# Performance work log

Hardware: AMD Instinct MI355X
Metric: run time of the kernel (lower is better)

Reference implementation:

```python
import jax, jax.numpy as jnp
import numpy as np

N, E, D = 100000, 1600000, 128
EPS = 1e-5


def _bn(h, g, b):
    m = h.mean(0)
    v = ((h - m) ** 2).mean(0)  # biased var, as torch BatchNorm1d normalization
    return g * (h - m) / jnp.sqrt(v + EPS) + b


def _sage(x, src, dst, w_self, w_neigh, b, n):
    # mean aggregation over in-neighbors (edges src->dst)
    agg = jax.ops.segment_sum(x[src], dst, num_segments=n)          # [N, D]
    cnt = jax.ops.segment_sum(jnp.ones(src.shape, x.dtype), dst, num_segments=n)
    mean = agg / jnp.maximum(cnt, 1.0)[:, None]
    return x @ w_self + mean @ w_neigh + b


def setup_inputs() -> dict:
    key = jax.random.key(0)
    ks = jax.random.split(key, 8)
    s = 1.0 / np.sqrt(D)
    return {
        "x": jax.random.normal(ks[0], (N, D), jnp.float32),
        "src": jax.random.randint(ks[1], (E,), 0, N, jnp.int32),
        "dst": jax.random.randint(ks[2], (E,), 0, N, jnp.int32),
        "w_self1": jax.random.normal(ks[3], (D, D), jnp.float32) * s,
        "w_neigh1": jax.random.normal(ks[4], (D, D), jnp.float32) * s,
        "b1": jnp.zeros((D,), jnp.float32),
        "w_self2": jax.random.normal(ks[5], (D, D), jnp.float32) * s,
        "w_neigh2": jax.random.normal(ks[6], (D, D), jnp.float32) * s,
        "b2": jnp.zeros((D,), jnp.float32),
        "w_skip": jax.random.normal(ks[7], (D, D), jnp.float32) * s,
        "b_skip": jnp.zeros((D,), jnp.float32),
        "g1": jnp.ones((D,), jnp.float32), "be1": jnp.zeros((D,), jnp.float32),
        "g2": jnp.ones((D,), jnp.float32), "be2": jnp.zeros((D,), jnp.float32),
        "g3": jnp.ones((D,), jnp.float32), "be3": jnp.zeros((D,), jnp.float32),
    }


def reference(x, src, dst, w_self1, w_neigh1, b1, w_self2, w_neigh2, b2,
              w_skip, b_skip, g1, be1, g2, be2, g3, be3):
    n = x.shape[0]
    h1 = _sage(x, src, dst, w_self1, w_neigh1, b1, n)
    h1 = jax.nn.relu(_bn(h1, g1, be1))           # dropout: eval-mode identity
    h2 = _sage(h1, src, dst, w_self2, w_neigh2, b2, n)
    h2 = _bn(h2, g2, be2)
    skip = _bn(h1 @ w_skip + b_skip, g3, be3)
    return jax.nn.relu(h2 + skip)
```

## Files before the change

### kernel.cpp

```cpp
#include <hip/hip_runtime.h>

#define D 128
#define PCHUNK 4096
#define SCAP 8192

typedef short bf16x8 __attribute__((ext_vector_type(8)));
typedef float f32x4 __attribute__((ext_vector_type(4)));

__device__ __forceinline__ ushort f2b(float f){
  unsigned u = __builtin_bit_cast(unsigned, f);
  u += 0x7fffu + ((u >> 16) & 1u);
  return (ushort)(u >> 16);
}
__device__ __forceinline__ float b2f(ushort h){
  unsigned u = ((unsigned)h) << 16;
  return __builtin_bit_cast(float, u);
}

__global__ __launch_bounds__(256) void k_p0(const int* __restrict__ dst,
                                            int* __restrict__ bcnt, int E){
  __shared__ int h[512];
  for (int u=threadIdx.x; u<512; u+=256) h[u]=0;
  __syncthreads();
  for (long long i=(long long)blockIdx.x*256+threadIdx.x; i<E; i+=(long long)gridDim.x*256)
    atomicAdd(&h[dst[i]>>8], 1);
  __syncthreads();
  for (int u=threadIdx.x; u<512; u+=256) if (h[u]) atomicAdd(&bcnt[u], h[u]);
}

__global__ void k_bscan(const int* __restrict__ bcnt, int* __restrict__ bbase,
                        int* __restrict__ bcur, int nb, int E){
  __shared__ int sh[1024];
  int t = threadIdx.x;
  int v = (t<nb) ? bcnt[t] : 0;
  sh[t]=v; __syncthreads();
  for (int off=1; off<1024; off<<=1){
    int add = (t>=off)?sh[t-off]:0;
    __syncthreads();
    sh[t]+=add;
    __syncthreads();
  }
  if (t<nb){ int e=sh[t]-v; bbase[t]=e; bcur[t]=e; }
  if (t==nb) bbase[t]=E;
}

__global__ __launch_bounds__(256) void k_part(const int* __restrict__ src,
        const int* __restrict__ dst, int* __restrict__ bcur,
        int2* __restrict__ pairs, int E){
  __shared__ int hist[512], offA[512], offB[512], gbase[512];
  __shared__ int sS[PCHUNK], sD[PCHUNK];
  const int t = threadIdx.x;
  const int base = blockIdx.x * PCHUNK;
  const int cnt = min(PCHUNK, E - base);
  for (int u=t; u<512; u+=256) hist[u]=0;
  __syncthreads();
  int rs[16], rd[16];
  #pragma unroll
  for (int j=0;j<16;j++){
    int li = j*256 + t;
    if (li < cnt){
      rs[j]=src[base+li]; rd[j]=dst[base+li];
      atomicAdd(&hist[rd[j]>>8],1);
    } else { rs[j]=0; rd[j]=-1; }
  }
  __syncthreads();
  int *cur=offA, *nxt=offB;
  for (int u=t; u<512; u+=256) cur[u]=hist[u];
  __syncthreads();
  for (int off=1; off<512; off<<=1){
    for (int u=t; u<512; u+=256) nxt[u] = cur[u] + ((u>=off)?cur[u-off]:0);
    __syncthreads();
    int* tmp=cur; cur=nxt; nxt=tmp;
  }
  for (int u=t; u<512; u+=256) nxt[u] = cur[u]-hist[u];
  __syncthreads();
  #pragma unroll
  for (int j=0;j<16;j++){
    if (j*256+t < cnt){
      int b = rd[j]>>8;
      int p = atomicAdd(&nxt[b],1);
      sS[p]=rs[j]; sD[p]=rd[j];
    }
  }
  __syncthreads();
  for (int u=t; u<512; u+=256){
    int c = hist[u];
    if (c>0) gbase[u] = atomicAdd(&bcur[u], c);
  }
  __syncthreads();
  #pragma unroll
  for (int j=0;j<16;j++){
    int idx = j*256+t;
    if (idx<cnt){
      int d = sD[idx]; int b = d>>8;
      int gpos = gbase[b] + (idx - (cur[b]-hist[b]));
      pairs[gpos] = make_int2(sS[idx], d);
    }
  }
}

__global__ __launch_bounds__(256) void k_sortb(const int2* __restrict__ pairs,
        const int* __restrict__ bbase, int* __restrict__ offs,
        int* __restrict__ slots, int N, int NB){
  __shared__ int nh[256], nc[256], sc[256];
  __shared__ int stage[SCAP];
  const int b = blockIdx.x, t = threadIdx.x;
  const int base = bbase[b];
  const int cnt  = bbase[b+1] - base;
  nh[t]=0; __syncthreads();
  for (int i=t;i<cnt;i+=256) atomicAdd(&nh[pairs[base+i].y & 255],1);
  __syncthreads();
  int v = nh[t];
  sc[t]=v; __syncthreads();
  for (int off=1; off<256; off<<=1){
    int add = (t>=off)?sc[t-off]:0;
    __syncthreads();
    sc[t]+=add;
    __syncthreads();
  }
  int excl = sc[t]-v;
  nc[t]=excl;
  int node = (b<<8)+t;
  if (node<N) offs[node]=base+excl;
  if (b==NB-1 && t==0) offs[N]=bbase[NB];
  __syncthreads();
  if (cnt<=SCAP){
    for (int i=t;i<cnt;i+=256){
      int2 p = pairs[base+i];
      int pos = atomicAdd(&nc[p.y & 255],1);
      stage[pos]=p.x;
    }
    __syncthreads();
    for (int i=t;i<cnt;i+=256) slots[base+i]=stage[i];
  } else {
    for (int i=t;i<cnt;i+=256){
      int2 p = pairs[base+i];
      int pos = atomicAdd(&nc[p.y & 255],1);
      slots[base+pos]=p.x;
    }
  }
}

__global__ __launch_bounds__(256) void k_xcast(const float* __restrict__ x,
                                               ushort* __restrict__ xb, long long n4){
  long long i = (long long)blockIdx.x*256 + threadIdx.x;
  const long long stride = (long long)gridDim.x*256;
  for (; i < n4; i += stride){
    float4 v = reinterpret_cast<const float4*>(x)[i];
    ushort4 o;
    o.x = f2b(v.x); o.y = f2b(v.y); o.z = f2b(v.z); o.w = f2b(v.w);
    reinterpret_cast<ushort4*>(xb)[i] = o;
  }
}

__global__ void k_wt(const float* __restrict__ W, ushort* __restrict__ Wb, int K, int k0){
  int idx = blockIdx.x*256 + threadIdx.x;
  int k = idx >> 7, c = idx & 127;
  Wb[(size_t)c*K + k0 + k] = f2b(W[idx]);
}

__global__ __launch_bounds__(256) void k_gatherb(const ushort* __restrict__ Xb,
        const int* __restrict__ slots, const int* __restrict__ offs,
        ushort* __restrict__ meanb, int N){
  int node = blockIdx.x*4 + (threadIdx.x >> 6);
  int c2 = (threadIdx.x & 63) * 2;
  if (node >= N) return;
  const int beg = offs[node], end = offs[node+1];
  float sx0=0,sy0=0,sx1=0,sy1=0,sx2=0,sy2=0,sx3=0,sy3=0;
  int j = beg;
  while (j < end && (j & 3)){
    unsigned u = *reinterpret_cast<const unsigned*>(&Xb[(size_t)slots[j]*D + c2]);
    sx0 += b2f((ushort)u); sy0 += b2f((ushort)(u>>16));
    ++j;
  }
  const int nfull = (end - j) >> 2;
  const int4* sp = reinterpret_cast<const int4*>(slots + j);

#define G8(ia, ib) { \
    unsigned u0 = *reinterpret_cast<const unsigned*>(&Xb[(size_t)(ia).x*D + c2]); \
    unsigned u1 = *reinterpret_cast<const unsigned*>(&Xb[(size_t)(ia).y*D + c2]); \
    unsigned u2 = *reinterpret_cast<const unsigned*>(&Xb[(size_t)(ia).z*D + c2]); \
    unsigned u3 = *reinterpret_cast<const unsigned*>(&Xb[(size_t)(ia).w*D + c2]); \
    unsigned u4 = *reinterpret_cast<const unsigned*>(&Xb[(size_t)(ib).x*D + c2]); \
    unsigned u5 = *reinterpret_cast<const unsigned*>(&Xb[(size_t)(ib).y*D + c2]); \
    unsigned u6 = *reinterpret_cast<const unsigned*>(&Xb[(size_t)(ib).z*D + c2]); \
    unsigned u7 = *reinterpret_cast<const unsigned*>(&Xb[(size_t)(ib).w*D + c2]); \
    sx0 += b2f((ushort)u0); sy0 += b2f((ushort)(u0>>16)); \
    sx1 += b2f((ushort)u1); sy1 += b2f((ushort)(u1>>16)); \
    sx2 += b2f((ushort)u2); sy2 += b2f((ushort)(u2>>16)); \
    sx3 += b2f((ushort)u3); sy3 += b2f((ushort)(u3>>16)); \
    sx0 += b2f((ushort)u4); sy0 += b2f((ushort)(u4>>16)); \
    sx1 += b2f((ushort)u5); sy1 += b2f((ushort)(u5>>16)); \
    sx2 += b2f((ushort)u6); sy2 += b2f((ushort)(u6>>16)); \
    sx3 += b2f((ushort)u7); sy3 += b2f((ushort)(u7>>16)); }

  int g = 0;
  if (nfull >= 2){
    int4 ia = sp[0], ib = sp[1];
    for (g = 2; g + 2 <= nfull; g += 2){
      int4 na = sp[g], nb = sp[g+1];
      G8(ia, ib);
      ia = na; ib = nb;
    }
    G8(ia, ib);
  }
  if (g < nfull){
    int4 ia = sp[g];
    unsigned u0 = *reinterpret_cast<const unsigned*>(&Xb[(size_t)ia.x*D + c2]);
    unsigned u1 = *reinterpret_cast<const unsigned*>(&Xb[(size_t)ia.y*D + c2]);
    unsigned u2 = *reinterpret_cast<const unsigned*>(&Xb[(size_t)ia.z*D + c2]);
    unsigned u3 = *reinterpret_cast<const unsigned*>(&Xb[(size_t)ia.w*D + c2]);
    sx0 += b2f((ushort)u0); sy0 += b2f((ushort)(u0>>16));
    sx1 += b2f((ushort)u1); sy1 += b2f((ushort)(u1>>16));
    sx2 += b2f((ushort)u2); sy2 += b2f((ushort)(u2>>16));
    sx3 += b2f((ushort)u3); sy3 += b2f((ushort)(u3>>16));
  }
  j += 4*nfull;
  for (; j < end; ++j){
    unsigned u = *reinterpret_cast<const unsigned*>(&Xb[(size_t)slots[j]*D + c2]);
    sx0 += b2f((ushort)u); sy0 += b2f((ushort)(u>>16));
  }
#undef G8
  float deg = (float)(end - beg);
  float rc = deg > 0.f ? 1.0f/deg : 0.f;
  unsigned o = (unsigned)f2b((sx0+sx1+sx2+sx3)*rc)
             | ((unsigned)f2b((sy0+sy1+sy2+sy3)*rc) << 16);
  *reinterpret_cast<unsigned*>(&meanb[(size_t)node*D + c2]) = o;
}

template<bool SKIP>
__global__ __launch_bounds__(256, 2) void k_mfma(
    const ushort* __restrict__ A0, const ushort* __restrict__ A1,
    const ushort* __restrict__ Wb, const ushort* __restrict__ Wk,
    const float* __restrict__ bias, const float* __restrict__ biasK,
    ushort* __restrict__ C, ushort* __restrict__ Ck,
    float* __restrict__ gS, float* __restrict__ gQ,
    float* __restrict__ gSK, float* __restrict__ gQK, int N, int NT)
{
  __shared__ ushort At[2][64][40];
  __shared__ ushort Wt[2][128][40];
  __shared__ ushort Wkt[SKIP ? 2*128*40 : 1];
  __shared__ float shS[128], shQ[128], shSK[SKIP?128:1], shQK[SKIP?128:1];
  const int tid = threadIdx.x;
  if (tid < 128){ shS[tid]=0.f; shQ[tid]=0.f; if (SKIP){ shSK[tid]=0.f; shQK[tid]=0.f; } }
  const int bid = blockIdx.x, gridN = gridDim.x;
  const int lane = tid & 63, wid = tid >> 6;
  const int wr = wid >> 1, wc = wid & 1;
  const int lr = lane & 15, kq = lane >> 4;
  const int srA = tid >> 2, s8A = (tid & 3) * 8;
  const int srW = tid >> 2, s8W = (tid & 3) * 8;

  int4 va0, va1, va2, va3;
  int4 w0a,w0b, w1a,w1b, w2a,w2b, w3a,w3b;
  int4 k0a,k0b, k1a,k1b, k2a,k2b, k3a,k3b;

#define LOADSET(S, GT, TT) { \
    int grow_ = (GT)*64 + srA; if (grow_ >= N) grow_ = N-1; \
    const ushort* As_ = ((TT) >= 4) ? A1 : A0; \
    va##S = *reinterpret_cast<const int4*>(&As_[(size_t)grow_*D + ((TT)&3)*32 + s8A]); \
    w##S##a = *reinterpret_cast<const int4*>(&Wb[(size_t)srW*256 + (TT)*32 + s8W]); \
    w##S##b = *reinterpret_cast<const int4*>(&Wb[(size_t)(srW+64)*256 + (TT)*32 + s8W]); \
    if (SKIP && (TT) < 4){ \
      k##S##a = *reinterpret_cast<const int4*>(&Wk[(size_t)srW*128 + (TT)*32 + s8W]); \
      k##S##b = *reinterpret_cast<const int4*>(&Wk[(size_t)(srW+64)*128 + (TT)*32 + s8W]); \
    } }

#define WRITESET(S, BW, TT) { \
    *reinterpret_cast<int4*>(&At[BW][srA][s8A]) = va##S; \
    *reinterpret_cast<int4*>(&Wt[BW][srW][s8W]) = w##S##a; \
    *reinterpret_cast<int4*>(&Wt[BW][srW+64][s8W]) = w##S##b; \
    if (SKIP && (TT) < 4){ \
      *reinterpret_cast<int4*>(&Wkt[((BW)*128 + srW)*40 + s8W]) = k##S##a; \
      *reinterpret_cast<int4*>(&Wkt[((BW)*128 + srW + 64)*40 + s8W]) = k##S##b; \
    } }

#define PBAR() { asm volatile("s_waitcnt lgkmcnt(0)" ::: "memory"); \
    __builtin_amdgcn_s_barrier(); __builtin_amdgcn_sched_barrier(0); }

#define STEPBODY(BR, WITHK, ...) { \
    bf16x8 af0 = *reinterpret_cast<const bf16x8*>(&At[BR][32*wr + lr][kq*8]); \
    bf16x8 af1 = *reinterpret_cast<const bf16x8*>(&At[BR][32*wr + 16 + lr][kq*8]); \
    bf16x8 bw0 = *reinterpret_cast<const bf16x8*>(&Wt[BR][64*wc + lr][kq*8]); \
    bf16x8 bw1 = *reinterpret_cast<const bf16x8*>(&Wt[BR][64*wc + 16 + lr][kq*8]); \
    bf16x8 bw2 = *reinterpret_cast<const bf16x8*>(&Wt[BR][64*wc + 32 + lr][kq*8]); \
    bf16x8 bw3 = *reinterpret_cast<const bf16x8*>(&Wt[BR][64*wc + 48 + lr][kq*8]); \
    bf16x8 bk0{}, bk1{}, bk2{}, bk3{}; \
    if (SKIP && (WITHK)){ \
      bk0 = *reinterpret_cast<const bf16x8*>(&Wkt[((BR)*128 + 64*wc + lr)*40 + kq*8]); \
      bk1 = *reinterpret_cast<const bf16x8*>(&Wkt[((BR)*128 + 64*wc + 16 + lr)*40 + kq*8]); \
      bk2 = *reinterpret_cast<const bf16x8*>(&Wkt[((BR)*128 + 64*wc + 32 + lr)*40 + kq*8]); \
      bk3 = *reinterpret_cast<const bf16x8*>(&Wkt[((BR)*128 + 64*wc + 48 + lr)*40 + kq*8]); \
    } \
    __VA_ARGS__; \
    acc[0][0] = __builtin_amdgcn_mfma_f32_16x16x32_bf16(af0, bw0, acc[0][0], 0,0,0); \
    acc[0][1] = __builtin_amdgcn_mfma_f32_16x16x32_bf16(af0, bw1, acc[0][1], 0,0,0); \
    acc[0][2] = __builtin_amdgcn_mfma_f32_16x16x32_bf16(af0, bw2, acc[0][2], 0,0,0); \
    acc[0][3] = __builtin_amdgcn_mfma_f32_16x16x32_bf16(af0, bw3, acc[0][3], 0,0,0); \
    acc[1][0] = __builtin_amdgcn_mfma_f32_16x16x32_bf16(af1, bw0, acc[1][0], 0,0,0); \
    acc[1][1] = __builtin_amdgcn_mfma_f32_16x16x32_bf16(af1, bw1, acc[1][1], 0,0,0); \
    acc[1][2] = __builtin_amdgcn_mfma_f32_16x16x32_bf16(af1, bw2, acc[1][2], 0,0,0); \
    acc[1][3] = __builtin_amdgcn_mfma_f32_16x16x32_bf16(af1, bw3, acc[1][3], 0,0,0); \
    if (SKIP && (WITHK)){ \
      accK[0][0] = __builtin_amdgcn_mfma_f32_16x16x32_bf16(af0, bk0, accK[0][0], 0,0,0); \
      accK[0][1] = __builtin_amdgcn_mfma_f32_16x16x32_bf16(af0, bk1, accK[0][1], 0,0,0); \
      accK[0][2] = __builtin_amdgcn_mfma_f32_16x16x32_bf16(af0, bk2, accK[0][2], 0,0,0); \
      accK[0][3] = __builtin_amdgcn_mfma_f32_16x16x32_bf16(af0, bk3, accK[0][3], 0,0,0); \
      accK[1][0] = __builtin_amdgcn_mfma_f32_16x16x32_bf16(af1, bk0, accK[1][0], 0,0,0); \
      accK[1][1] = __builtin_amdgcn_mfma_f32_16x16x32_bf16(af1, bk1, accK[1][1], 0,0,0); \
      accK[1][2] = __builtin_amdgcn_mfma_f32_16x16x32_bf16(af1, bk2, accK[1][2], 0,0,0); \
      accK[1][3] = __builtin_amdgcn_mfma_f32_16x16x32_bf16(af1, bk3, accK[1][3], 0,0,0); \
    } }

  f32x4 acc[2][4], accK[SKIP?2:1][SKIP?4:1];
  #pragma unroll
  for (int m=0;m<2;m++)
    #pragma unroll
    for (int n=0;n<4;n++){
      acc[m][n] = (f32x4){0.f,0.f,0.f,0.f};
      if (SKIP) accK[m][n] = (f32x4){0.f,0.f,0.f,0.f};
    }
  float bs[4]={0,0,0,0}, bq[4]={0,0,0,0}, bsk[4]={0,0,0,0}, bqk[4]={0,0,0,0};
  float bv[4], bkv[4];
  #pragma unroll
  for (int n=0;n<4;n++){
    bv[n] = bias[64*wc + 16*n + lr];
    bkv[n] = SKIP ? biasK[64*wc + 16*n + lr] : 0.f;
  }

  {
    const int t0 = bid;
    LOADSET(0, t0, 0);
    LOADSET(1, t0, 1);
    LOADSET(2, t0, 2);
    LOADSET(3, t0, 3);
    WRITESET(0, 0, 0);
    PBAR();
  }

  for (int tile = bid; tile < NT; tile += gridN){
    const int tnext = tile + gridN;
    const bool hasnext = (tnext < NT);
    STEPBODY(0, 1, LOADSET(0, tile, 4));
    WRITESET(1, 1, 1); PBAR();
    STEPBODY(1, 1, LOADSET(1, tile, 5));
    WRITESET(2, 0, 2); PBAR();
    STEPBODY(0, 1, LOADSET(2, tile, 6));
    WRITESET(3, 1, 3); PBAR();
    STEPBODY(1, 1, LOADSET(3, tile, 7));
    WRITESET(0, 0, 4); PBAR();
    STEPBODY(0, 0, if (hasnext) LOADSET(0, tnext, 0));
    WRITESET(1, 1, 5); PBAR();
    STEPBODY(1, 0, if (hasnext) LOADSET(1, tnext, 1));
    WRITESET(2, 0, 6); PBAR();
    STEPBODY(0, 0, if (hasnext) LOADSET(2, tnext, 2));
    WRITESET(3, 1, 7); PBAR();
    STEPBODY(1, 0, if (hasnext) LOADSET(3, tnext, 3));
    if (hasnext){ WRITESET(0, 0, 0); PBAR(); }

    #pragma unroll
    for (int m=0;m<2;m++){
      #pragma unroll
      for (int r=0;r<4;r++){
        int row = tile*64 + 32*wr + 16*m + kq*4 + r;
        if (row < N){
          #pragma unroll
          for (int n=0;n<4;n++){
            int col = 64*wc + 16*n + lr;
            float v = acc[m][n][r] + bv[n];
            C[(size_t)row*D + col] = f2b(v);
            bs[n] += v; bq[n] += v*v;
            if (SKIP){
              float u = accK[m][n][r] + bkv[n];
              Ck[(size_t)row*D + col] = f2b(u);
              bsk[n] += u; bqk[n] += u*u;
            }
          }
        }
      }
    }
    #pragma unroll
    for (int m=0;m<2;m++)
      #pragma unroll
      for (int n=0;n<4;n++){
        acc[m][n] = (f32x4){0.f,0.f,0.f,0.f};
        if (SKIP) accK[m][n] = (f32x4){0.f,0.f,0.f,0.f};
      }
  }
#undef LOADSET
#undef WRITESET
#undef PBAR
#undef STEPBODY

  #pragma unroll
  for (int n=0;n<4;n++){
    float s = bs[n], q = bq[n];
    s += __shfl_xor(s,16); s += __shfl_xor(s,32);
    q += __shfl_xor(q,16); q += __shfl_xor(q,32);
    if (kq == 0){
      int col = 64*wc + 16*n + lr;
      atomicAdd(&shS[col], s);
      atomicAdd(&shQ[col], q);
    }
    if (SKIP){
      float sk = bsk[n], qk = bqk[n];
      sk += __shfl_xor(sk,16); sk += __shfl_xor(sk,32);
      qk += __shfl_xor(qk,16); qk += __shfl_xor(qk,32);
      if (kq == 0){
        int col = 64*wc + 16*n + lr;
        atomicAdd(&shSK[col], sk);
        atomicAdd(&shQK[col], qk);
      }
    }
  }
  __syncthreads();
  if (tid < 128){
    unsafeAtomicAdd(&gS[tid], shS[tid]);
    unsafeAtomicAdd(&gQ[tid], shQ[tid]);
    if (SKIP){
      unsafeAtomicAdd(&gSK[tid], shSK[tid]);
      unsafeAtomicAdd(&gQK[tid], shQK[tid]);
    }
  }
}

__global__ void k_bnfin(const float* __restrict__ sum, const float* __restrict__ sq,
                        const float* __restrict__ g, const float* __restrict__ be,
                        float* __restrict__ bnA, float* __restrict__ bnB, float invN){
  int c = threadIdx.x;
  float m = sum[c]*invN;
  float v = sq[c]*invN - m*m;
  float a = g[c]*rsqrtf(fmaxf(v, 0.f) + 1e-5f);
  bnA[c] = a;
  bnB[c] = be[c] - m*a;
}

__global__ __launch_bounds__(256) void k_bnrelub(const ushort* __restrict__ hpre,
      ushort* __restrict__ hb,
      const float* __restrict__ A, const float* __restrict__ Bp, long long n4){
  long long i = (long long)blockIdx.x*256 + threadIdx.x;
  const long long stride = (long long)gridDim.x*256;
  for (; i < n4; i += stride){
    int c = ((int)(i & 31)) << 2;
    float4 a = *reinterpret_cast<const float4*>(A + c);
    float4 b = *reinterpret_cast<const float4*>(Bp + c);
    ushort4 hv = reinterpret_cast<const ushort4*>(hpre)[i];
    ushort4 o;
    o.x = f2b(fmaxf(a.x*b2f(hv.x) + b.x, 0.f));
    o.y = f2b(fmaxf(a.y*b2f(hv.y) + b.y, 0.f));
    o.z = f2b(fmaxf(a.z*b2f(hv.z) + b.z, 0.f));
    o.w = f2b(fmaxf(a.w*b2f(hv.w) + b.w, 0.f));
    reinterpret_cast<ushort4*>(hb)[i] = o;
  }
}

__global__ __launch_bounds__(256) void k_final(const ushort* __restrict__ h2,
      const ushort* __restrict__ sk, float* __restrict__ out,
      const float* __restrict__ A2, const float* __restrict__ B2,
      const float* __restrict__ A3, const float* __restrict__ B3, long long n4){
  long long i = (long long)blockIdx.x*256 + threadIdx.x;
  const long long stride = (long long)gridDim.x*256;
  for (; i < n4; i += stride){
    int c = ((int)(i & 31)) << 2;
    float4 a2 = *reinterpret_cast<const float4*>(A2 + c);
    float4 b2 = *reinterpret_cast<const float4*>(B2 + c);
    float4 a3 = *reinterpret_cast<const float4*>(A3 + c);
    float4 b3 = *reinterpret_cast<const float4*>(B3 + c);
    ushort4 h = reinterpret_cast<const ushort4*>(h2)[i];
    ushort4 s = reinterpret_cast<const ushort4*>(sk)[i];
    float4 v;
    v.x = fmaxf(a2.x*b2f(h.x) + b2.x + a3.x*b2f(s.x) + b3.x, 0.f);
    v.y = fmaxf(a2.y*b2f(h.y) + b2.y + a3.y*b2f(s.y) + b3.y, 0.f);
    v.z = fmaxf(a2.z*b2f(h.z) + b2.z + a3.z*b2f(s.z) + b3.z, 0.f);
    v.w = fmaxf(a2.w*b2f(h.w) + b2.w + a3.w*b2f(s.w) + b3.w, 0.f);
    reinterpret_cast<float4*>(out)[i] = v;
  }
}

extern "C" void kernel_launch(void* const* d_in, const int* in_sizes, int n_in,
                              void* d_out, int out_size, void* d_ws, size_t ws_size,
                              hipStream_t stream) {
  const float* x        = (const float*)d_in[0];
  const int*   src      = (const int*)  d_in[1];
  const int*   dst      = (const int*)  d_in[2];
  const float* w_self1  = (const float*)d_in[3];
  const float* w_neigh1 = (const float*)d_in[4];
  const float* b1       = (const float*)d_in[5];
  const float* w_self2  = (const float*)d_in[6];
  const float* w_neigh2 = (const float*)d_in[7];
  const float* b2       = (const float*)d_in[8];
  const float* w_skip   = (const float*)d_in[9];
  const float* b_skip   = (const float*)d_in[10];
  const float* g1       = (const float*)d_in[11];
  const float* be1      = (const float*)d_in[12];
  const float* g2       = (const float*)d_in[13];
  const float* be2      = (const float*)d_in[14];
  const float* g3       = (const float*)d_in[15];
  const float* be3      = (const float*)d_in[16];
  (void)n_in; (void)ws_size;

  const int N = in_sizes[0] / D;
  const int E = in_sizes[1];
  const int NB = (N + 255) >> 8;
  float* out = (float*)d_out;

  char* p = (char*)d_ws;
  const size_t nd2 = (((size_t)N * D * 2) + 255) / 256 * 256;
  ushort* meanb  = (ushort*)p; p += nd2;
  ushort* h1b    = (ushort*)p; p += nd2;
  ushort* hpre_b = (ushort*)p; p += nd2;
  ushort* skip_b = (ushort*)p; p += nd2;
  ushort* Wb1    = (ushort*)p; p += 256*128*2;
  ushort* Wb2    = (ushort*)p; p += 256*128*2;
  ushort* Wb3    = (ushort*)p; p += 128*128*2;
  int*    offs   = (int*)p;   p += (((size_t)(N+1)*4) + 255) / 256 * 256;
  int*    bcnt   = (int*)p;   p += 2304;
  float*  st     = (float*)p; p += 1536*sizeof(float);
  int*    bbase  = (int*)p;   p += 2304;
  int*    bcur   = (int*)p;   p += 2048;
  float *sum1=st,      *sq1=st+128,  *sum2=st+256, *sq2=st+384, *sum3=st+512, *sq3=st+640;
  float *bnA1=st+768,  *bnB1=st+896, *bnA2=st+1024,*bnB2=st+1152,*bnA3=st+1280,*bnB3=st+1408;

  const size_t slpad = (((size_t)E*4) + 255) / 256 * 256;
  const size_t xbpad = (((size_t)N*D*2) + 255) / 256 * 256;
  int*    slots = (int*)d_out;
  ushort* xb    = (ushort*)((char*)d_out + slpad);
  int2*   pairs = (int2*)((char*)d_out + slpad + xbpad);

  hipMemsetAsync(bcnt, 0, 2304 + 1536*sizeof(float), stream);

  const long long n4 = (long long)N * D / 4;

  k_xcast<<<2048, 256, 0, stream>>>(x, xb, n4);
  k_wt<<<64, 256, 0, stream>>>(w_self1,  Wb1, 256, 0);
  k_wt<<<64, 256, 0, stream>>>(w_neigh1, Wb1, 256, 128);
  k_wt<<<64, 256, 0, stream>>>(w_self2,  Wb2, 256, 0);
  k_wt<<<64, 256, 0, stream>>>(w_neigh2, Wb2, 256, 128);
  k_wt<<<64, 256, 0, stream>>>(w_skip,   Wb3, 128, 0);

  k_p0<<<1024, 256, 0, stream>>>(dst, bcnt, E);
  k_bscan<<<1, 1024, 0, stream>>>(bcnt, bbase, bcur, NB, E);
  k_part<<<(E + PCHUNK - 1)/PCHUNK, 256, 0, stream>>>(src, dst, bcur, pairs, E);
  k_sortb<<<NB, 256, 0, stream>>>(pairs, bbase, offs, slots, N, NB);

  const int gablocks = (N + 3) / 4;
  const int NT = (N + 63) / 64;
  const int gpersist = 512;
  const float invN = 1.0f / (float)N;

  k_gatherb<<<gablocks, 256, 0, stream>>>(xb, slots, offs, meanb, N);
  k_mfma<false><<<gpersist, 256, 0, stream>>>(xb, meanb, Wb1, nullptr, b1, nullptr,
                                              hpre_b, nullptr, sum1, sq1, nullptr, nullptr, N, NT);
  k_bnfin<<<1, 128, 0, stream>>>(sum1, sq1, g1, be1, bnA1, bnB1, invN);
  k_bnrelub<<<4096, 256, 0, stream>>>(hpre_b, h1b, bnA1, bnB1, n4);

  k_gatherb<<<gablocks, 256, 0, stream>>>(h1b, slots, offs, meanb, N);

  k_mfma<true><<<gpersist, 256, 0, stream>>>(h1b, meanb, Wb2, Wb3, b2, b_skip,
                                             hpre_b, skip_b, sum2, sq2, sum3, sq3, N, NT);
  k_bnfin<<<1, 128, 0, stream>>>(sum2, sq2, g2, be2, bnA2, bnB2, invN);
  k_bnfin<<<1, 128, 0, stream>>>(sum3, sq3, g3, be3, bnA3, bnB3, invN);

  k_final<<<4096, 256, 0, stream>>>(hpre_b, skip_b, out, bnA2, bnB2, bnA3, bnB3, n4);
}
```

Before: 315.8 us.

## Pack edge pairs into 32-bit words and deepen gather software pipeline

Partition pairs now store the source index with the low 8 bits of dst in the top byte of a single 32-bit word, halving the pair buffer traffic in the partition and bucket-sort kernels. The gather kernel is restructured to load 8 neighbor indices per step with double-buffered register sets, issuing the next batch of loads before accumulating the previous one, and uses 8 packed f32x2 accumulators with 32-bit index arithmetic. This trades higher register use for more memory-level parallelism. Packing assumes node ids fit in 24 bits.

```diff
diff --git a/kernel.cpp b/kernel.cpp
--- a/kernel.cpp
+++ b/kernel.cpp
@@ -6,6 +6,7 @@
 
 typedef short bf16x8 __attribute__((ext_vector_type(8)));
 typedef float f32x4 __attribute__((ext_vector_type(4)));
+typedef float f32x2 __attribute__((ext_vector_type(2)));
 
 __device__ __forceinline__ ushort f2b(float f){
   unsigned u = __builtin_bit_cast(unsigned, f);
@@ -15,6 +16,12 @@
 __device__ __forceinline__ float b2f(ushort h){
   unsigned u = ((unsigned)h) << 16;
   return __builtin_bit_cast(float, u);
+}
+__device__ __forceinline__ f32x2 upk(unsigned u){
+  f32x2 r;
+  r.x = __builtin_bit_cast(float, u << 16);
+  r.y = __builtin_bit_cast(float, u & 0xffff0000u);
+  return r;
 }
 
 __global__ __launch_bounds__(256) void k_p0(const int* __restrict__ dst,
@@ -46,7 +53,7 @@
 
 __global__ __launch_bounds__(256) void k_part(const int* __restrict__ src,
         const int* __restrict__ dst, int* __restrict__ bcur,
-        int2* __restrict__ pairs, int E){
+        unsigned* __restrict__ pairs, int E){
   __shared__ int hist[512], offA[512], offB[512], gbase[512];
   __shared__ int sS[PCHUNK], sD[PCHUNK];
   const int t = threadIdx.x;
@@ -94,12 +101,12 @@
     if (idx<cnt){
       int d = sD[idx]; int b = d>>8;
       int gpos = gbase[b] + (idx - (cur[b]-hist[b]));
-      pairs[gpos] = make_int2(sS[idx], d);
-    }
-  }
-}
-
-__global__ __launch_bounds__(256) void k_sortb(const int2* __restrict__ pairs,
+      pairs[gpos] = (unsigned)sS[idx] | ((unsigned)(d & 255) << 24);
+    }
+  }
+}
+
+__global__ __launch_bounds__(256) void k_sortb(const unsigned* __restrict__ pairs,
         const int* __restrict__ bbase, int* __restrict__ offs,
         int* __restrict__ slots, int N, int NB){
   __shared__ int nh[256], nc[256], sc[256];
@@ -108,7 +115,7 @@
   const int base = bbase[b];
   const int cnt  = bbase[b+1] - base;
   nh[t]=0; __syncthreads();
-  for (int i=t;i<cnt;i+=256) atomicAdd(&nh[pairs[base+i].y & 255],1);
+  for (int i=t;i<cnt;i+=256) atomicAdd(&nh[pairs[base+i] >> 24],1);
   __syncthreads();
   int v = nh[t];
   sc[t]=v; __syncthreads();
@@ -126,17 +133,17 @@
   __syncthreads();
   if (cnt<=SCAP){
     for (int i=t;i<cnt;i+=256){
-      int2 p = pairs[base+i];
-      int pos = atomicAdd(&nc[p.y & 255],1);
-      stage[pos]=p.x;
+      unsigned p = pairs[base+i];
+      int pos = atomicAdd(&nc[p >> 24],1);
+      stage[pos]=(int)(p & 0xffffffu);
     }
     __syncthreads();
     for (int i=t;i<cnt;i+=256) slots[base+i]=stage[i];
   } else {
     for (int i=t;i<cnt;i+=256){
-      int2 p = pairs[base+i];
-      int pos = atomicAdd(&nc[p.y & 255],1);
-      slots[base+pos]=p.x;
+      unsigned p = pairs[base+i];
+      int pos = atomicAdd(&nc[p >> 24],1);
+      slots[base+pos]=(int)(p & 0xffffffu);
     }
   }
 }
@@ -163,69 +170,67 @@
         const int* __restrict__ slots, const int* __restrict__ offs,
         ushort* __restrict__ meanb, int N){
   int node = blockIdx.x*4 + (threadIdx.x >> 6);
-  int c2 = (threadIdx.x & 63) * 2;
+  const unsigned c2 = (threadIdx.x & 63) * 2;
   if (node >= N) return;
   const int beg = offs[node], end = offs[node+1];
-  float sx0=0,sy0=0,sx1=0,sy1=0,sx2=0,sy2=0,sx3=0,sy3=0;
+  f32x2 s0{0,0},s1{0,0},s2{0,0},s3{0,0},s4{0,0},s5{0,0},s6{0,0},s7{0,0};
   int j = beg;
   while (j < end && (j & 3)){
-    unsigned u = *reinterpret_cast<const unsigned*>(&Xb[(size_t)slots[j]*D + c2]);
-    sx0 += b2f((ushort)u); sy0 += b2f((ushort)(u>>16));
+    s0 += upk(*reinterpret_cast<const unsigned*>(Xb + ((unsigned)slots[j]*128u + c2)));
     ++j;
   }
-  const int nfull = (end - j) >> 2;
+  const int nfull = (end - j) >> 3;
   const int4* sp = reinterpret_cast<const int4*>(slots + j);
 
-#define G8(ia, ib) { \
-    unsigned u0 = *reinterpret_cast<const unsigned*>(&Xb[(size_t)(ia).x*D + c2]); \
-    unsigned u1 = *reinterpret_cast<const unsigned*>(&Xb[(size_t)(ia).y*D + c2]); \
-    unsigned u2 = *reinterpret_cast<const unsigned*>(&Xb[(size_t)(ia).z*D + c2]); \
-    unsigned u3 = *reinterpret_cast<const unsigned*>(&Xb[(size_t)(ia).w*D + c2]); \
-    unsigned u4 = *reinterpret_cast<const unsigned*>(&Xb[(size_t)(ib).x*D + c2]); \
-    unsigned u5 = *reinterpret_cast<const unsigned*>(&Xb[(size_t)(ib).y*D + c2]); \
-    unsigned u6 = *reinterpret_cast<const unsigned*>(&Xb[(size_t)(ib).z*D + c2]); \
-    unsigned u7 = *reinterpret_cast<const unsigned*>(&Xb[(size_t)(ib).w*D + c2]); \
-    sx0 += b2f((ushort)u0); sy0 += b2f((ushort)(u0>>16)); \
-    sx1 += b2f((ushort)u1); sy1 += b2f((ushort)(u1>>16)); \
-    sx2 += b2f((ushort)u2); sy2 += b2f((ushort)(u2>>16)); \
-    sx3 += b2f((ushort)u3); sy3 += b2f((ushort)(u3>>16)); \
-    sx0 += b2f((ushort)u4); sy0 += b2f((ushort)(u4>>16)); \
-    sx1 += b2f((ushort)u5); sy1 += b2f((ushort)(u5>>16)); \
-    sx2 += b2f((ushort)u6); sy2 += b2f((ushort)(u6>>16)); \
-    sx3 += b2f((ushort)u7); sy3 += b2f((ushort)(u7>>16)); }
-
-  int g = 0;
-  if (nfull >= 2){
+#define GLD(dstv, idx) dstv = *reinterpret_cast<const unsigned*>(Xb + ((unsigned)(idx)*128u + c2))
+#define GATHER8(U, ia, ib) \
+    GLD(U##0, (ia).x); GLD(U##1, (ia).y); GLD(U##2, (ia).z); GLD(U##3, (ia).w); \
+    GLD(U##4, (ib).x); GLD(U##5, (ib).y); GLD(U##6, (ib).z); GLD(U##7, (ib).w)
+#define ACC8(U) \
+    s0 += upk(U##0); s1 += upk(U##1); s2 += upk(U##2); s3 += upk(U##3); \
+    s4 += upk(U##4); s5 += upk(U##5); s6 += upk(U##6); s7 += upk(U##7)
+
+  unsigned a0,a1,a2,a3,a4,a5,a6,a7;
+  unsigned b0,b1,b2,b3,b4,b5,b6,b7;
+  if (nfull > 0){
     int4 ia = sp[0], ib = sp[1];
-    for (g = 2; g + 2 <= nfull; g += 2){
-      int4 na = sp[g], nb = sp[g+1];
-      G8(ia, ib);
-      ia = na; ib = nb;
-    }
-    G8(ia, ib);
-  }
-  if (g < nfull){
-    int4 ia = sp[g];
-    unsigned u0 = *reinterpret_cast<const unsigned*>(&Xb[(size_t)ia.x*D + c2]);
-    unsigned u1 = *reinterpret_cast<const unsigned*>(&Xb[(size_t)ia.y*D + c2]);
-    unsigned u2 = *reinterpret_cast<const unsigned*>(&Xb[(size_t)ia.z*D + c2]);
-    unsigned u3 = *reinterpret_cast<const unsigned*>(&Xb[(size_t)ia.w*D + c2]);
-    sx0 += b2f((ushort)u0); sy0 += b2f((ushort)(u0>>16));
-    sx1 += b2f((ushort)u1); sy1 += b2f((ushort)(u1>>16));
-    sx2 += b2f((ushort)u2); sy2 += b2f((ushort)(u2>>16));
-    sx3 += b2f((ushort)u3); sy3 += b2f((ushort)(u3>>16));
-  }
-  j += 4*nfull;
-  for (; j < end; ++j){
-    unsigned u = *reinterpret_cast<const unsigned*>(&Xb[(size_t)slots[j]*D + c2]);
-    sx0 += b2f((ushort)u); sy0 += b2f((ushort)(u>>16));
-  }
-#undef G8
+    GATHER8(a, ia, ib);
+    int g = 1;
+    if (nfull > 1){ ia = sp[2]; ib = sp[3]; }
+    for (; g + 1 < nfull; g += 2){
+      GATHER8(b, ia, ib);
+      ia = sp[2*g+2]; ib = sp[2*g+3];
+      ACC8(a);
+      GATHER8(a, ia, ib);
+      if (g + 2 < nfull){ ia = sp[2*g+4]; ib = sp[2*g+5]; }
+      ACC8(b);
+    }
+    if (g < nfull){
+      GATHER8(b, ia, ib);
+      ACC8(a);
+      ACC8(b);
+    } else {
+      ACC8(a);
+    }
+  }
+  j += 8*nfull;
+  if (end - j >= 4){
+    int4 ia = *reinterpret_cast<const int4*>(slots + j);
+    unsigned t0,t1,t2,t3;
+    GLD(t0, ia.x); GLD(t1, ia.y); GLD(t2, ia.z); GLD(t3, ia.w);
+    s0 += upk(t0); s1 += upk(t1); s2 += upk(t2); s3 += upk(t3);
+    j += 4;
+  }
+  for (; j < end; ++j)
+    s0 += upk(*reinterpret_cast<const unsigned*>(Xb + ((unsigned)slots[j]*128u + c2)));
+#undef GLD
+#undef GATHER8
+#undef ACC8
+  f32x2 s = ((s0+s1)+(s2+s3)) + ((s4+s5)+(s6+s7));
   float deg = (float)(end - beg);
   float rc = deg > 0.f ? 1.0f/deg : 0.f;
-  unsigned o = (unsigned)f2b((sx0+sx1+sx2+sx3)*rc)
-             | ((unsigned)f2b((sy0+sy1+sy2+sy3)*rc) << 16);
-  *reinterpret_cast<unsigned*>(&meanb[(size_t)node*D + c2]) = o;
+  unsigned o = (unsigned)f2b(s.x*rc) | ((unsigned)f2b(s.y*rc) << 16);
+  *reinterpret_cast<unsigned*>(meanb + ((size_t)node*D + c2)) = o;
 }
 
 template<bool SKIP>
@@ -522,9 +527,9 @@
 
   const size_t slpad = (((size_t)E*4) + 255) / 256 * 256;
   const size_t xbpad = (((size_t)N*D*2) + 255) / 256 * 256;
-  int*    slots = (int*)d_out;
-  ushort* xb    = (ushort*)((char*)d_out + slpad);
-  int2*   pairs = (int2*)((char*)d_out + slpad + xbpad);
+  int*      slots = (int*)d_out;
+  ushort*   xb    = (ushort*)((char*)d_out + slpad);
+  unsigned* pairs = (unsigned*)((char*)d_out + slpad + xbpad);
 
   hipMemsetAsync(bcnt, 0, 2304 + 1536*sizeof(float), stream);
 
```

Measured after the change: 343.6 us. +8.8%, slower.

## Pack edge pairs into 32 bits and use 128-row MFMA tiles, splitting skip GEMM

Applied to the files above, without the earlier changes.

Edge partition pairs are packed into one 32-bit word (src in the low 24 bits, dst low byte in the high 8), which halves the traffic of the intermediate pair buffer between partition and bucket sort. The GEMM kernel now uses 128-row tiles with a 4x4 accumulator grid per wave, so each weight tile loaded into shared memory is reused across more rows. The fused skip projection in the second layer is split into a separate K=128 GEMM launch, which re-reads h1 but lowers register and LDS pressure in the main kernel. Packing assumes node ids fit in 24 bits, and the larger tiles raise register use under the 2-blocks-per-CU launch bound.

```diff
diff --git a/kernel.cpp b/kernel.cpp
--- a/kernel.cpp
+++ b/kernel.cpp
@@ -46,7 +46,7 @@
 
 __global__ __launch_bounds__(256) void k_part(const int* __restrict__ src,
         const int* __restrict__ dst, int* __restrict__ bcur,
-        int2* __restrict__ pairs, int E){
+        unsigned* __restrict__ pairs, int E){
   __shared__ int hist[512], offA[512], offB[512], gbase[512];
   __shared__ int sS[PCHUNK], sD[PCHUNK];
   const int t = threadIdx.x;
@@ -94,12 +94,12 @@
     if (idx<cnt){
       int d = sD[idx]; int b = d>>8;
       int gpos = gbase[b] + (idx - (cur[b]-hist[b]));
-      pairs[gpos] = make_int2(sS[idx], d);
-    }
-  }
-}
-
-__global__ __launch_bounds__(256) void k_sortb(const int2* __restrict__ pairs,
+      pairs[gpos] = (unsigned)sS[idx] | ((unsigned)(d & 255) << 24);
+    }
+  }
+}
+
+__global__ __launch_bounds__(256) void k_sortb(const unsigned* __restrict__ pairs,
         const int* __restrict__ bbase, int* __restrict__ offs,
         int* __restrict__ slots, int N, int NB){
   __shared__ int nh[256], nc[256], sc[256];
@@ -108,7 +108,7 @@
   const int base = bbase[b];
   const int cnt  = bbase[b+1] - base;
   nh[t]=0; __syncthreads();
-  for (int i=t;i<cnt;i+=256) atomicAdd(&nh[pairs[base+i].y & 255],1);
+  for (int i=t;i<cnt;i+=256) atomicAdd(&nh[pairs[base+i] >> 24],1);
   __syncthreads();
   int v = nh[t];
   sc[t]=v; __syncthreads();
@@ -126,17 +126,17 @@
   __syncthreads();
   if (cnt<=SCAP){
     for (int i=t;i<cnt;i+=256){
-      int2 p = pairs[base+i];
-      int pos = atomicAdd(&nc[p.y & 255],1);
-      stage[pos]=p.x;
+      unsigned p = pairs[base+i];
+      int pos = atomicAdd(&nc[p >> 24],1);
+      stage[pos]=(int)(p & 0xffffffu);
     }
     __syncthreads();
     for (int i=t;i<cnt;i+=256) slots[base+i]=stage[i];
   } else {
     for (int i=t;i<cnt;i+=256){
-      int2 p = pairs[base+i];
-      int pos = atomicAdd(&nc[p.y & 255],1);
-      slots[base+pos]=p.x;
+      unsigned p = pairs[base+i];
+      int pos = atomicAdd(&nc[p >> 24],1);
+      slots[base+pos]=(int)(p & 0xffffffu);
     }
   }
 }
@@ -228,69 +228,56 @@
   *reinterpret_cast<unsigned*>(&meanb[(size_t)node*D + c2]) = o;
 }
 
-template<bool SKIP>
+template<int KS>
 __global__ __launch_bounds__(256, 2) void k_mfma(
     const ushort* __restrict__ A0, const ushort* __restrict__ A1,
-    const ushort* __restrict__ Wb, const ushort* __restrict__ Wk,
-    const float* __restrict__ bias, const float* __restrict__ biasK,
-    ushort* __restrict__ C, ushort* __restrict__ Ck,
-    float* __restrict__ gS, float* __restrict__ gQ,
-    float* __restrict__ gSK, float* __restrict__ gQK, int N, int NT)
+    const ushort* __restrict__ Wb, const float* __restrict__ bias,
+    ushort* __restrict__ C, float* __restrict__ gS, float* __restrict__ gQ,
+    int N, int NT)
 {
-  __shared__ ushort At[2][64][40];
+  constexpr int KW = KS * 32;
+  __shared__ ushort At[2][128][40];
   __shared__ ushort Wt[2][128][40];
-  __shared__ ushort Wkt[SKIP ? 2*128*40 : 1];
-  __shared__ float shS[128], shQ[128], shSK[SKIP?128:1], shQK[SKIP?128:1];
+  __shared__ float shS[128], shQ[128];
   const int tid = threadIdx.x;
-  if (tid < 128){ shS[tid]=0.f; shQ[tid]=0.f; if (SKIP){ shSK[tid]=0.f; shQK[tid]=0.f; } }
+  if (tid < 128){ shS[tid]=0.f; shQ[tid]=0.f; }
   const int bid = blockIdx.x, gridN = gridDim.x;
   const int lane = tid & 63, wid = tid >> 6;
   const int wr = wid >> 1, wc = wid & 1;
   const int lr = lane & 15, kq = lane >> 4;
-  const int srA = tid >> 2, s8A = (tid & 3) * 8;
-  const int srW = tid >> 2, s8W = (tid & 3) * 8;
-
-  int4 va0, va1, va2, va3;
+  const int sr = tid >> 2, s8 = (tid & 3) * 8;
+
+  int4 a0a,a0b, a1a,a1b, a2a,a2b, a3a,a3b;
   int4 w0a,w0b, w1a,w1b, w2a,w2b, w3a,w3b;
-  int4 k0a,k0b, k1a,k1b, k2a,k2b, k3a,k3b;
 
 #define LOADSET(S, GT, TT) { \
-    int grow_ = (GT)*64 + srA; if (grow_ >= N) grow_ = N-1; \
-    const ushort* As_ = ((TT) >= 4) ? A1 : A0; \
-    va##S = *reinterpret_cast<const int4*>(&As_[(size_t)grow_*D + ((TT)&3)*32 + s8A]); \
-    w##S##a = *reinterpret_cast<const int4*>(&Wb[(size_t)srW*256 + (TT)*32 + s8W]); \
-    w##S##b = *reinterpret_cast<const int4*>(&Wb[(size_t)(srW+64)*256 + (TT)*32 + s8W]); \
-    if (SKIP && (TT) < 4){ \
-      k##S##a = *reinterpret_cast<const int4*>(&Wk[(size_t)srW*128 + (TT)*32 + s8W]); \
-      k##S##b = *reinterpret_cast<const int4*>(&Wk[(size_t)(srW+64)*128 + (TT)*32 + s8W]); \
-    } }
-
-#define WRITESET(S, BW, TT) { \
-    *reinterpret_cast<int4*>(&At[BW][srA][s8A]) = va##S; \
-    *reinterpret_cast<int4*>(&Wt[BW][srW][s8W]) = w##S##a; \
-    *reinterpret_cast<int4*>(&Wt[BW][srW+64][s8W]) = w##S##b; \
-    if (SKIP && (TT) < 4){ \
-      *reinterpret_cast<int4*>(&Wkt[((BW)*128 + srW)*40 + s8W]) = k##S##a; \
-      *reinterpret_cast<int4*>(&Wkt[((BW)*128 + srW + 64)*40 + s8W]) = k##S##b; \
-    } }
+    int gr0_ = (GT)*128 + sr;      if (gr0_ >= N) gr0_ = N-1; \
+    int gr1_ = (GT)*128 + sr + 64; if (gr1_ >= N) gr1_ = N-1; \
+    const ushort* As_ = (KS == 8 && (TT) >= 4) ? A1 : A0; \
+    const int ka_ = ((TT) & 3) * 32; \
+    a##S##a = *reinterpret_cast<const int4*>(&As_[(size_t)gr0_*D + ka_ + s8]); \
+    a##S##b = *reinterpret_cast<const int4*>(&As_[(size_t)gr1_*D + ka_ + s8]); \
+    w##S##a = *reinterpret_cast<const int4*>(&Wb[(size_t)sr*KW + (TT)*32 + s8]); \
+    w##S##b = *reinterpret_cast<const int4*>(&Wb[(size_t)(sr+64)*KW + (TT)*32 + s8]); }
+
+#define WRITESET(S, BW) { \
+    *reinterpret_cast<int4*>(&At[BW][sr][s8]) = a##S##a; \
+    *reinterpret_cast<int4*>(&At[BW][sr+64][s8]) = a##S##b; \
+    *reinterpret_cast<int4*>(&Wt[BW][sr][s8]) = w##S##a; \
+    *reinterpret_cast<int4*>(&Wt[BW][sr+64][s8]) = w##S##b; }
 
 #define PBAR() { asm volatile("s_waitcnt lgkmcnt(0)" ::: "memory"); \
     __builtin_amdgcn_s_barrier(); __builtin_amdgcn_sched_barrier(0); }
 
-#define STEPBODY(BR, WITHK, ...) { \
-    bf16x8 af0 = *reinterpret_cast<const bf16x8*>(&At[BR][32*wr + lr][kq*8]); \
-    bf16x8 af1 = *reinterpret_cast<const bf16x8*>(&At[BR][32*wr + 16 + lr][kq*8]); \
+#define STEPBODY(BR, ...) { \
+    bf16x8 af0 = *reinterpret_cast<const bf16x8*>(&At[BR][64*wr + lr][kq*8]); \
+    bf16x8 af1 = *reinterpret_cast<const bf16x8*>(&At[BR][64*wr + 16 + lr][kq*8]); \
+    bf16x8 af2 = *reinterpret_cast<const bf16x8*>(&At[BR][64*wr + 32 + lr][kq*8]); \
+    bf16x8 af3 = *reinterpret_cast<const bf16x8*>(&At[BR][64*wr + 48 + lr][kq*8]); \
     bf16x8 bw0 = *reinterpret_cast<const bf16x8*>(&Wt[BR][64*wc + lr][kq*8]); \
     bf16x8 bw1 = *reinterpret_cast<const bf16x8*>(&Wt[BR][64*wc + 16 + lr][kq*8]); \
     bf16x8 bw2 = *reinterpret_cast<const bf16x8*>(&Wt[BR][64*wc + 32 + lr][kq*8]); \
     bf16x8 bw3 = *reinterpret_cast<const bf16x8*>(&Wt[BR][64*wc + 48 + lr][kq*8]); \
-    bf16x8 bk0{}, bk1{}, bk2{}, bk3{}; \
-    if (SKIP && (WITHK)){ \
-      bk0 = *reinterpret_cast<const bf16x8*>(&Wkt[((BR)*128 + 64*wc + lr)*40 + kq*8]); \
-      bk1 = *reinterpret_cast<const bf16x8*>(&Wkt[((BR)*128 + 64*wc + 16 + lr)*40 + kq*8]); \
-      bk2 = *reinterpret_cast<const bf16x8*>(&Wkt[((BR)*128 + 64*wc + 32 + lr)*40 + kq*8]); \
-      bk3 = *reinterpret_cast<const bf16x8*>(&Wkt[((BR)*128 + 64*wc + 48 + lr)*40 + kq*8]); \
-    } \
     __VA_ARGS__; \
     acc[0][0] = __builtin_amdgcn_mfma_f32_16x16x32_bf16(af0, bw0, acc[0][0], 0,0,0); \
     acc[0][1] = __builtin_amdgcn_mfma_f32_16x16x32_bf16(af0, bw1, acc[0][1], 0,0,0); \
@@ -300,32 +287,24 @@
     acc[1][1] = __builtin_amdgcn_mfma_f32_16x16x32_bf16(af1, bw1, acc[1][1], 0,0,0); \
     acc[1][2] = __builtin_amdgcn_mfma_f32_16x16x32_bf16(af1, bw2, acc[1][2], 0,0,0); \
     acc[1][3] = __builtin_amdgcn_mfma_f32_16x16x32_bf16(af1, bw3, acc[1][3], 0,0,0); \
-    if (SKIP && (WITHK)){ \
-      accK[0][0] = __builtin_amdgcn_mfma_f32_16x16x32_bf16(af0, bk0, accK[0][0], 0,0,0); \
-      accK[0][1] = __builtin_amdgcn_mfma_f32_16x16x32_bf16(af0, bk1, accK[0][1], 0,0,0); \
-      accK[0][2] = __builtin_amdgcn_mfma_f32_16x16x32_bf16(af0, bk2, accK[0][2], 0,0,0); \
-      accK[0][3] = __builtin_amdgcn_mfma_f32_16x16x32_bf16(af0, bk3, accK[0][3], 0,0,0); \
-      accK[1][0] = __builtin_amdgcn_mfma_f32_16x16x32_bf16(af1, bk0, accK[1][0], 0,0,0); \
-      accK[1][1] = __builtin_amdgcn_mfma_f32_16x16x32_bf16(af1, bk1, accK[1][1], 0,0,0); \
-      accK[1][2] = __builtin_amdgcn_mfma_f32_16x16x32_bf16(af1, bk2, accK[1][2], 0,0,0); \
-      accK[1][3] = __builtin_amdgcn_mfma_f32_16x16x32_bf16(af1, bk3, accK[1][3], 0,0,0); \
-    } }
-
-  f32x4 acc[2][4], accK[SKIP?2:1][SKIP?4:1];
+    acc[2][0] = __builtin_amdgcn_mfma_f32_16x16x32_bf16(af2, bw0, acc[2][0], 0,0,0); \
+    acc[2][1] = __builtin_amdgcn_mfma_f32_16x16x32_bf16(af2, bw1, acc[2][1], 0,0,0); \
+    acc[2][2] = __builtin_amdgcn_mfma_f32_16x16x32_bf16(af2, bw2, acc[2][2], 0,0,0); \
+    acc[2][3] = __builtin_amdgcn_mfma_f32_16x16x32_bf16(af2, bw3, acc[2][3], 0,0,0); \
+    acc[3][0] = __builtin_amdgcn_mfma_f32_16x16x32_bf16(af3, bw0, acc[3][0], 0,0,0); \
+    acc[3][1] = __builtin_amdgcn_mfma_f32_16x16x32_bf16(af3, bw1, acc[3][1], 0,0,0); \
+    acc[3][2] = __builtin_amdgcn_mfma_f32_16x16x32_bf16(af3, bw2, acc[3][2], 0,0,0); \
+    acc[3][3] = __builtin_amdgcn_mfma_f32_16x16x32_bf16(af3, bw3, acc[3][3], 0,0,0); }
+
+  f32x4 acc[4][4];
   #pragma unroll
-  for (int m=0;m<2;m++)
+  for (int m=0;m<4;m++)
     #pragma unroll
-    for (int n=0;n<4;n++){
-      acc[m][n] = (f32x4){0.f,0.f,0.f,0.f};
-      if (SKIP) accK[m][n] = (f32x4){0.f,0.f,0.f,0.f};
-    }
-  float bs[4]={0,0,0,0}, bq[4]={0,0,0,0}, bsk[4]={0,0,0,0}, bqk[4]={0,0,0,0};
-  float bv[4], bkv[4];
+    for (int n=0;n<4;n++) acc[m][n] = (f32x4){0.f,0.f,0.f,0.f};
+  float bs[4]={0,0,0,0}, bq[4]={0,0,0,0};
+  float bv[4];
   #pragma unroll
-  for (int n=0;n<4;n++){
-    bv[n] = bias[64*wc + 16*n + lr];
-    bkv[n] = SKIP ? biasK[64*wc + 16*n + lr] : 0.f;
-  }
+  for (int n=0;n<4;n++) bv[n] = bias[64*wc + 16*n + lr];
 
   {
     const int t0 = bid;
@@ -333,35 +312,46 @@
     LOADSET(1, t0, 1);
     LOADSET(2, t0, 2);
     LOADSET(3, t0, 3);
-    WRITESET(0, 0, 0);
+    WRITESET(0, 0);
     PBAR();
   }
 
   for (int tile = bid; tile < NT; tile += gridN){
     const int tnext = tile + gridN;
     const bool hasnext = (tnext < NT);
-    STEPBODY(0, 1, LOADSET(0, tile, 4));
-    WRITESET(1, 1, 1); PBAR();
-    STEPBODY(1, 1, LOADSET(1, tile, 5));
-    WRITESET(2, 0, 2); PBAR();
-    STEPBODY(0, 1, LOADSET(2, tile, 6));
-    WRITESET(3, 1, 3); PBAR();
-    STEPBODY(1, 1, LOADSET(3, tile, 7));
-    WRITESET(0, 0, 4); PBAR();
-    STEPBODY(0, 0, if (hasnext) LOADSET(0, tnext, 0));
-    WRITESET(1, 1, 5); PBAR();
-    STEPBODY(1, 0, if (hasnext) LOADSET(1, tnext, 1));
-    WRITESET(2, 0, 6); PBAR();
-    STEPBODY(0, 0, if (hasnext) LOADSET(2, tnext, 2));
-    WRITESET(3, 1, 7); PBAR();
-    STEPBODY(1, 0, if (hasnext) LOADSET(3, tnext, 3));
-    if (hasnext){ WRITESET(0, 0, 0); PBAR(); }
+    if (KS == 8){
+      STEPBODY(0, LOADSET(0, tile, 4));
+      WRITESET(1, 1); PBAR();
+      STEPBODY(1, LOADSET(1, tile, 5));
+      WRITESET(2, 0); PBAR();
+      STEPBODY(0, LOADSET(2, tile, 6));
+      WRITESET(3, 1); PBAR();
+      STEPBODY(1, LOADSET(3, tile, 7));
+      WRITESET(0, 0); PBAR();
+      STEPBODY(0, if (hasnext) LOADSET(0, tnext, 0));
+      WRITESET(1, 1); PBAR();
+      STEPBODY(1, if (hasnext) LOADSET(1, tnext, 1));
+      WRITESET(2, 0); PBAR();
+      STEPBODY(0, if (hasnext) LOADSET(2, tnext, 2));
+      WRITESET(3, 1); PBAR();
+      STEPBODY(1, if (hasnext) LOADSET(3, tnext, 3));
+      if (hasnext){ WRITESET(0, 0); PBAR(); }
+    } else {
+      STEPBODY(0, if (hasnext) LOADSET(0, tnext, 0));
+      WRITESET(1, 1); PBAR();
+      STEPBODY(1, if (hasnext) LOADSET(1, tnext, 1));
+      WRITESET(2, 0); PBAR();
+      STEPBODY(0, if (hasnext) LOADSET(2, tnext, 2));
+      WRITESET(3, 1); PBAR();
+      STEPBODY(1, if (hasnext) LOADSET(3, tnext, 3));
+      if (hasnext){ WRITESET(0, 0); PBAR(); }
+    }
 
     #pragma unroll
-    for (int m=0;m<2;m++){
+    for (int m=0;m<4;m++){
       #pragma unroll
       for (int r=0;r<4;r++){
-        int row = tile*64 + 32*wr + 16*m + kq*4 + r;
+        int row = tile*128 + 64*wr + 16*m + kq*4 + r;
         if (row < N){
           #pragma unroll
           for (int n=0;n<4;n++){
@@ -369,22 +359,14 @@
             float v = acc[m][n][r] + bv[n];
             C[(size_t)row*D + col] = f2b(v);
             bs[n] += v; bq[n] += v*v;
-            if (SKIP){
-              float u = accK[m][n][r] + bkv[n];
-              Ck[(size_t)row*D + col] = f2b(u);
-              bsk[n] += u; bqk[n] += u*u;
-            }
           }
         }
       }
     }
     #pragma unroll
-    for (int m=0;m<2;m++)
+    for (int m=0;m<4;m++)
       #pragma unroll
-      for (int n=0;n<4;n++){
-        acc[m][n] = (f32x4){0.f,0.f,0.f,0.f};
-        if (SKIP) accK[m][n] = (f32x4){0.f,0.f,0.f,0.f};
-      }
+      for (int n=0;n<4;n++) acc[m][n] = (f32x4){0.f,0.f,0.f,0.f};
   }
 #undef LOADSET
 #undef WRITESET
@@ -401,25 +383,11 @@
       atomicAdd(&shS[col], s);
       atomicAdd(&shQ[col], q);
     }
-    if (SKIP){
-      float sk = bsk[n], qk = bqk[n];
-      sk += __shfl_xor(sk,16); sk += __shfl_xor(sk,32);
-      qk += __shfl_xor(qk,16); qk += __shfl_xor(qk,32);
-      if (kq == 0){
-        int col = 64*wc + 16*n + lr;
-        atomicAdd(&shSK[col], sk);
-        atomicAdd(&shQK[col], qk);
-      }
-    }
   }
   __syncthreads();
   if (tid < 128){
     unsafeAtomicAdd(&gS[tid], shS[tid]);
     unsafeAtomicAdd(&gQ[tid], shQ[tid]);
-    if (SKIP){
-      unsafeAtomicAdd(&gSK[tid], shSK[tid]);
-      unsafeAtomicAdd(&gQK[tid], shQK[tid]);
-    }
   }
 }
 
@@ -522,9 +490,9 @@
 
   const size_t slpad = (((size_t)E*4) + 255) / 256 * 256;
   const size_t xbpad = (((size_t)N*D*2) + 255) / 256 * 256;
-  int*    slots = (int*)d_out;
-  ushort* xb    = (ushort*)((char*)d_out + slpad);
-  int2*   pairs = (int2*)((char*)d_out + slpad + xbpad);
+  int*      slots = (int*)d_out;
+  ushort*   xb    = (ushort*)((char*)d_out + slpad);
+  unsigned* pairs = (unsigned*)((char*)d_out + slpad + xbpad);
 
   hipMemsetAsync(bcnt, 0, 2304 + 1536*sizeof(float), stream);
 
@@ -543,20 +511,19 @@
   k_sortb<<<NB, 256, 0, stream>>>(pairs, bbase, offs, slots, N, NB);
 
   const int gablocks = (N + 3) / 4;
-  const int NT = (N + 63) / 64;
+  const int NT = (N + 127) / 128;
   const int gpersist = 512;
   const float invN = 1.0f / (float)N;
 
   k_gatherb<<<gablocks, 256, 0, stream>>>(xb, slots, offs, meanb, N);
-  k_mfma<false><<<gpersist, 256, 0, stream>>>(xb, meanb, Wb1, nullptr, b1, nullptr,
-                                              hpre_b, nullptr, sum1, sq1, nullptr, nullptr, N, NT);
+  k_mfma<8><<<gpersist, 256, 0, stream>>>(xb, meanb, Wb1, b1, hpre_b, sum1, sq1, N, NT);
   k_bnfin<<<1, 128, 0, stream>>>(sum1, sq1, g1, be1, bnA1, bnB1, invN);
   k_bnrelub<<<4096, 256, 0, stream>>>(hpre_b, h1b, bnA1, bnB1, n4);
 
   k_gatherb<<<gablocks, 256, 0, stream>>>(h1b, slots, offs, meanb, N);
 
-  k_mfma<true><<<gpersist, 256, 0, stream>>>(h1b, meanb, Wb2, Wb3, b2, b_skip,
-                                             hpre_b, skip_b, sum2, sq2, sum3, sq3, N, NT);
+  k_mfma<8><<<gpersist, 256, 0, stream>>>(h1b, meanb, Wb2, b2, hpre_b, sum2, sq2, N, NT);
+  k_mfma<4><<<gpersist, 256, 0, stream>>>(h1b, nullptr, Wb3, b_skip, skip_b, sum3, sq3, N, NT);
   k_bnfin<<<1, 128, 0, stream>>>(sum2, sq2, g2, be2, bnA2, bnB2, invN);
   k_bnfin<<<1, 128, 0, stream>>>(sum3, sq3, g3, be3, bnA3, bnB3, invN);
 
```

Result: slower. 329.8 us (+4.4%).
